# Performance work log

Hardware: AMD Instinct MI355X
Metric: run time of the kernel (lower is better)

The kernel has to match this reference:

```python
import jax, jax.numpy as jnp
import numpy as np

ALPHA = 1.702  # gpt-oss gated-activation alpha
LIMIT = 7.0    # gpt-oss clamp limit
E, H, I = 8, 1024, 2048
B, S = 2, 2048


def setup_inputs() -> dict:
    key = jax.random.key(0)
    ks = jax.random.split(key, 6)
    return {
        "hidden_states": jax.random.normal(ks[0], (B, S, H), dtype=jnp.float32),
        "routing_weights": jax.random.uniform(ks[1], (B * S, E), dtype=jnp.float32),
        "gate_up_proj": jax.random.normal(ks[2], (E, H, 2 * I), dtype=jnp.float32) * 0.02,
        "gate_up_proj_bias": jax.random.normal(ks[3], (E, 2 * I), dtype=jnp.float32) * 0.02,
        "down_proj": jax.random.normal(ks[4], (E, I, H), dtype=jnp.float32) * 0.02,
        "down_proj_bias": jax.random.normal(ks[5], (E, H), dtype=jnp.float32) * 0.02,
    }


def reference(hidden_states, routing_weights, gate_up_proj, gate_up_proj_bias,
              down_proj, down_proj_bias):
    b, s, h = hidden_states.shape
    x = hidden_states.reshape(-1, h)  # [T, H]
    # all-experts dense path: [E, T, 2I]
    gate_up = jnp.einsum('th,ehd->etd', x, gate_up_proj) + gate_up_proj_bias[:, None, :]
    gate = gate_up[..., ::2]   # interleaved gate/up as in gpt-oss
    up = gate_up[..., 1::2]
    gate = jnp.minimum(gate, LIMIT)
    up = jnp.clip(up, -LIMIT, LIMIT)
    glu = gate * jax.nn.sigmoid(gate * ALPHA)
    # [E, T, H]
    out_e = jnp.einsum('eti,eih->eth', (up + 1.0) * glu, down_proj) + down_proj_bias[:, None, :]
    # weighted sum over experts with routing weights [T, E]
    out = jnp.einsum('eth,te->th', out_e, routing_weights)
    return out.reshape(b, s, h)
```

## Files before the change

### kernel.cpp

```cpp
#include <hip/hip_runtime.h>
#include <cstdint>

#define E_  8
#define H_  1024
#define I_  2048
#define T_  4096
#define D2_ 4096
#define K2_ 16384

typedef __bf16 bf16x8 __attribute__((ext_vector_type(8)));
typedef float  f32x4  __attribute__((ext_vector_type(4)));

__device__ __forceinline__ unsigned short f2bf(float f) {
  unsigned int u = __float_as_uint(f);
  u += 0x7FFFu + ((u >> 16) & 1u);
  return (unsigned short)(u >> 16);
}

__device__ __forceinline__ void gll16(const void* g, void* l) {
  __builtin_amdgcn_global_load_lds(
      (const __attribute__((address_space(1))) unsigned int*)(uintptr_t)g,
      (__attribute__((address_space(3))) unsigned int*)(uintptr_t)l,
      16, 0, 0);
}

#define BARX()  __builtin_amdgcn_s_barrier()
#define FENCE() __builtin_amdgcn_sched_barrier(0)
#define LGK0()  asm volatile("s_waitcnt lgkmcnt(0)" ::: "memory")
#define WVM0()  asm volatile("s_waitcnt vmcnt(0)" ::: "memory")

__global__ void cast_x_kernel(const float* __restrict__ x,
                              unsigned short* __restrict__ xb) {
  const int idx = (blockIdx.x * 256 + threadIdx.x) * 8;
  float4 a = *(const float4*)(x + idx);
  float4 b = *(const float4*)(x + idx + 4);
  unsigned short o[8];
  o[0]=f2bf(a.x); o[1]=f2bf(a.y); o[2]=f2bf(a.z); o[3]=f2bf(a.w);
  o[4]=f2bf(b.x); o[5]=f2bf(b.y); o[6]=f2bf(b.z); o[7]=f2bf(b.w);
  *(uint4*)(xb + idx) = *(const uint4*)o;
}

__global__ void transp_w1_kernel(const float* __restrict__ gup,
                                 unsigned short* __restrict__ w1g,
                                 unsigned short* __restrict__ w1u) {
  __shared__ float tile[64][65];
  const int h0 = blockIdx.x * 64;
  const int d0 = blockIdx.y * 64;
  const int e  = blockIdx.z;
  const int tid = threadIdx.x;
  const int r  = tid >> 4;
  const int c4 = (tid & 15) * 4;
  const float* src = gup + ((size_t)e * H_ + h0) * D2_ + d0;
#pragma unroll
  for (int c = 0; c < 4; ++c) {
    const int row = r + 16 * c;
    float4 v = *(const float4*)(src + (size_t)row * D2_ + c4);
    tile[row][c4+0] = v.x; tile[row][c4+1] = v.y;
    tile[row][c4+2] = v.z; tile[row][c4+3] = v.w;
  }
  __syncthreads();
  const int hl = tid & 63;
  const int jg = tid >> 6;
  const size_t jbase = (size_t)e * I_ + (d0 >> 1);
#pragma unroll
  for (int jj = 0; jj < 8; ++jj) {
    const int jl = jg * 8 + jj;
    w1g[(jbase + jl) * H_ + h0 + hl] = f2bf(tile[hl][2*jl]);
    w1u[(jbase + jl) * H_ + h0 + hl] = f2bf(tile[hl][2*jl+1]);
  }
}

__global__ void transp_w2_kernel(const float* __restrict__ dp,
                                 unsigned short* __restrict__ w2t) {
  __shared__ float tile[64][65];
  const int k0 = blockIdx.x * 64;
  const int h0 = blockIdx.y * 64;
  const int tid = threadIdx.x;
  const int r  = tid >> 4;
  const int c4 = (tid & 15) * 4;
#pragma unroll
  for (int c = 0; c < 4; ++c) {
    const int row = r + 16 * c;
    float4 v = *(const float4*)(dp + (size_t)(k0 + row) * H_ + h0 + c4);
    tile[row][c4+0] = v.x; tile[row][c4+1] = v.y;
    tile[row][c4+2] = v.z; tile[row][c4+3] = v.w;
  }
  __syncthreads();
  const int kl = tid & 63;
  const int hg = tid >> 6;
#pragma unroll
  for (int hh = 0; hh < 16; ++hh) {
    const int hl = hg * 16 + hh;
    w2t[(size_t)(h0 + hl) * K2_ + k0 + kl] = f2bf(tile[kl][hl]);
  }
}


#define STA1(B, HF, KT) {                                                    \
  _Pragma("unroll")                                                           \
  for (int ld = 0; ld < 2; ++ld) {                                            \
    const int r = rA + (HF)*64 + ld*128;                                      \
    gll16(Ag + (size_t)r * H_ + (KT)*64 + sg, &lds[B][r*64 + sl]);            \
  } }
#define STG1(B, KT) {                                                         \
  _Pragma("unroll")                                                           \
  for (int ld = 0; ld < 2; ++ld) {                                            \
    const int r = rA + ld*64;                                                 \
    gll16(Gg + (size_t)r * H_ + (KT)*64 + sg, &lds[B][16384 + r*64 + sl]);    \
  } }
#define STU1(B, KT) {                                                         \
  _Pragma("unroll")                                                           \
  for (int ld = 0; ld < 2; ++ld) {                                            \
    const int r = rA + ld*64;                                                 \
    gll16(Ug + (size_t)r * H_ + (KT)*64 + sg, &lds[B][24576 + r*64 + sl]);    \
  } }
#define LDA1(B, MH) {                                                         \
  _Pragma("unroll")                                                           \
  for (int m = 0; m < 4; ++m) {                                               \
    const int ro = (wm*128 + (MH)*64 + m*16 + arow) * 64;                     \
    av[m][0] = *(const bf16x8*)&lds[B][ro + sw0];                             \
    av[m][1] = *(const bf16x8*)&lds[B][ro + sw1];                             \
  } }
#define LDB1(B, DST, BASE) {                                                  \
  _Pragma("unroll")                                                           \
  for (int n = 0; n < 2; ++n) {                                               \
    const int ro = (BASE) + (wn*32 + n*16 + arow) * 64;                       \
    DST[n][0] = *(const bf16x8*)&lds[B][ro + sw0];                            \
    DST[n][1] = *(const bf16x8*)&lds[B][ro + sw1];                            \
  } }
#define MMA1(ACC, MH, BV)                                                     \
  __builtin_amdgcn_s_setprio(1);                                              \
  _Pragma("unroll")                                                           \
  for (int m = 0; m < 4; ++m)                                                 \
  _Pragma("unroll")                                                           \
  for (int n = 0; n < 2; ++n) {                                               \
    ACC[(MH)*4+m][n] = __builtin_amdgcn_mfma_f32_16x16x32_bf16(av[m][0], BV[n][0], ACC[(MH)*4+m][n], 0,0,0); \
    ACC[(MH)*4+m][n] = __builtin_amdgcn_mfma_f32_16x16x32_bf16(av[m][1], BV[n][1], ACC[(MH)*4+m][n], 0,0,0); \
  }                                                                           \
  __builtin_amdgcn_s_setprio(0);

#define NT1 16
#define TILE1(B, U) {                                                         \
                \
  if ((U)+1 < NT1) { STA1((B)^1, 0, (U)+1); STA1((B)^1, 1, (U)+1);            \
                     STG1((B)^1, (U)+1);    STU1((B)^1, (U)+1); }             \
  FENCE();                          \
  LDA1(B, 0); LDB1(B, bgv, 16384); LDB1(B, buv, 24576);                       \
  MMA1(accg, 0, bgv); MMA1(accu, 0, buv);                                     \
  LDA1(B, 1);                                                                 \
  MMA1(accu, 1, buv); MMA1(accg, 1, bgv);                                     \
  LGK0();                      \
  if ((U)+1 < NT1) WVM0();       \
  BARX();                                                                     \
  FENCE();                                   \
}

__global__ __launch_bounds__(512, 2) void gemm1_act_kernel(
    const unsigned short* __restrict__ xb,
    const unsigned short* __restrict__ w1g,
    const unsigned short* __restrict__ w1u,
    const float* __restrict__ gub,
    const float* __restrict__ rw,
    unsigned short* __restrict__ actW)
{
  __shared__ unsigned short lds[2][32768];
  const int tid  = threadIdx.x;
  const int lane = tid & 63;
  const int wv   = tid >> 6;
  const int wm   = wv >> 2;
  const int wn   = wv & 3;

  const int L  = blockIdx.x + 16 * blockIdx.y;
  const int xk = L & 7, xs = L >> 3;
  const int t0 = ((xk >> 1) * 4 + (xs & 3)) * 256;
  const int j0 = ((xk & 1) * 8 + (xs >> 2)) * 128;
  const int e  = blockIdx.z;

  const int arow = lane & 15;
  const int q    = lane >> 4;
  const int sw0  = ((q    ) ^ (arow & 7)) * 8;
  const int sw1  = ((q + 4) ^ (arow & 7)) * 8;
  const int sg   = ((tid & 7) ^ ((tid >> 3) & 7)) * 8;
  const int sl   = (tid & 7) * 8;
  const int rA   = tid >> 3;

  const unsigned short* Ag = xb  + (size_t)t0 * H_;
  const unsigned short* Gg = w1g + ((size_t)e * I_ + j0) * H_;
  const unsigned short* Ug = w1u + ((size_t)e * I_ + j0) * H_;

  const f32x4 zero = {0.f, 0.f, 0.f, 0.f};
  f32x4 accg[8][2], accu[8][2];
#pragma unroll
  for (int m = 0; m < 8; ++m)
#pragma unroll
    for (int n = 0; n < 2; ++n) { accg[m][n] = zero; accu[m][n] = zero; }
  bf16x8 av[4][2], bgv[2][2], buv[2][2];

  STA1(0, 0, 0); STA1(0, 1, 0); STG1(0, 0); STU1(0, 0);
  WVM0(); BARX(); FENCE();

#pragma unroll 1
  for (int t = 0; t < NT1; t += 2) {
    TILE1(0, t);
    TILE1(1, t+1);
  }

  const float* gbE = gub + (size_t)e * D2_;
#pragma unroll
  for (int n = 0; n < 2; ++n) {
    const int j = j0 + wn*32 + n*16 + arow;
    const float2 bgu = *(const float2*)&gbE[2*j];
#pragma unroll
    for (int mf = 0; mf < 8; ++mf) {
#pragma unroll
      for (int ri = 0; ri < 4; ++ri) {
        const int t = t0 + wm*128 + mf*16 + q*4 + ri;
        float g = accg[mf][n][ri] + bgu.x;
        float u = accu[mf][n][ri] + bgu.y;
        g = fminf(g, 7.0f);
        u = fminf(fmaxf(u, -7.0f), 7.0f);
        const float s   = 1.0f / (1.0f + __expf(-1.702f * g));
        const float val = (u + 1.0f) * (g * s) * rw[t * 8 + e];
        actW[(size_t)t * K2_ + e * I_ + j] = f2bf(val);
      }
    }
  }
}


#define STA2(B, HF, KT) {                                                    \
  _Pragma("unroll")                                                           \
  for (int ld = 0; ld < 2; ++ld) {                                            \
    const int r = rA + (HF)*64 + ld*128;                                      \
    gll16(Ag + (size_t)r * K2_ + (KT)*64 + sg, &lds[B][r*64 + sl]);           \
  } }
#define STB2(B, NH, KT) {                                                    \
  _Pragma("unroll")                                                           \
  for (int ld = 0; ld < 2; ++ld) {                                            \
    const int lr = rA + ld*64;                                                \
    const int r  = (lr & 31) + (NH)*32 + ((lr >> 5) << 6);                    \
    gll16(Bgp + (size_t)r * K2_ + (KT)*64 + sg, &lds[B][16384 + r*64 + sl]);  \
  } }
#define LDA2(B, MH) {                                                         \
  _Pragma("unroll")                                                           \
  for (int m = 0; m < 4; ++m) {                                               \
    const int ro = (wm*128 + (MH)*64 + m*16 + arow) * 64;                     \
    av[m][0] = *(const bf16x8*)&lds[B][ro + sw0];                             \
    av[m][1] = *(const bf16x8*)&lds[B][ro + sw1];                             \
  } }
#define LDB2(B, DST, NH) {                                                   \
  _Pragma("unroll")                                                           \
  for (int n = 0; n < 2; ++n) {                                               \
    const int ro = 16384 + (wn*64 + (NH)*32 + n*16 + arow) * 64;              \
    DST[n][0] = *(const bf16x8*)&lds[B][ro + sw0];                            \
    DST[n][1] = *(const bf16x8*)&lds[B][ro + sw1];                            \
  } }
#define MMA2(MH, NH, BV)                                                      \
  __builtin_amdgcn_s_setprio(1);                                              \
  _Pragma("unroll")                                                           \
  for (int m = 0; m < 4; ++m)                                                 \
  _Pragma("unroll")                                                           \
  for (int n = 0; n < 2; ++n) {                                               \
    acc[(MH)*4+m][(NH)*2+n] = __builtin_amdgcn_mfma_f32_16x16x32_bf16(av[m][0], BV[n][0], acc[(MH)*4+m][(NH)*2+n], 0,0,0); \
    acc[(MH)*4+m][(NH)*2+n] = __builtin_amdgcn_mfma_f32_16x16x32_bf16(av[m][1], BV[n][1], acc[(MH)*4+m][(NH)*2+n], 0,0,0); \
  }                                                                           \
  __builtin_amdgcn_s_setprio(0);

#define NT2 64
#define TILE2(B, U) {                                                         \
  if ((U)+1 < NT2) { STA2((B)^1, 0, (U)+1); STA2((B)^1, 1, (U)+1);            \
                     STB2((B)^1, 0, (U)+1); STB2((B)^1, 1, (U)+1); }          \
  FENCE();                                                                    \
  LDA2(B, 0); LDB2(B, bv0, 0); LDB2(B, bv1, 1);                               \
  MMA2(0, 0, bv0); MMA2(0, 1, bv1);                                           \
  LDA2(B, 1);                                                                 \
  MMA2(1, 0, bv0); MMA2(1, 1, bv1);                                           \
  LGK0();                                                                     \
  if ((U)+1 < NT2) WVM0();                                                    \
  BARX();                                                                     \
  FENCE();                                                                    \
}

__global__ __launch_bounds__(512, 2) void gemm2_kernel(
    const unsigned short* __restrict__ actW,
    const unsigned short* __restrict__ w2t,
    float* __restrict__ part)
{
  __shared__ unsigned short lds[2][32768];
  const int tid  = threadIdx.x;
  const int lane = tid & 63;
  const int wv   = tid >> 6;
  const int wm   = wv >> 2;
  const int wn   = wv & 3;

  const int L  = blockIdx.x + 16 * (blockIdx.y + 4 * blockIdx.z);
  const int xk = L & 7, xs = L >> 3;
  const int t0 = ((xk & 1) * 8 + (xs & 7)) * 256;
  const int h0 = (xs >> 3) * 256;
  const int cz = xk >> 1;
  const int c0 = cz * 4096;

  const int arow = lane & 15;
  const int q    = lane >> 4;
  const int sw0  = ((q    ) ^ (arow & 7)) * 8;
  const int sw1  = ((q + 4) ^ (arow & 7)) * 8;
  const int sg   = ((tid & 7) ^ ((tid >> 3) & 7)) * 8;
  const int sl   = (tid & 7) * 8;
  const int rA   = tid >> 3;

  const unsigned short* Ag  = actW + (size_t)t0 * K2_ + c0;
  const unsigned short* Bgp = w2t  + (size_t)h0 * K2_ + c0;

  const f32x4 zero = {0.f, 0.f, 0.f, 0.f};
  f32x4 acc[8][4];
#pragma unroll
  for (int m = 0; m < 8; ++m)
#pragma unroll
    for (int n = 0; n < 4; ++n) acc[m][n] = zero;
  bf16x8 av[4][2], bv0[2][2], bv1[2][2];

  STA2(0, 0, 0); STA2(0, 1, 0); STB2(0, 0, 0); STB2(0, 1, 0);
  WVM0(); BARX(); FENCE();

#pragma unroll 1
  for (int t = 0; t < NT2; t += 2) {
    TILE2(0, t);
    TILE2(1, t+1);
  }

  float* P = part + (size_t)cz * ((size_t)T_ * H_);
#pragma unroll
  for (int mf = 0; mf < 8; ++mf)
#pragma unroll
    for (int nf = 0; nf < 4; ++nf)
#pragma unroll
      for (int ri = 0; ri < 4; ++ri) {
        const int t = t0 + wm*128 + mf*16 + q*4 + ri;
        const int h = h0 + wn*64 + nf*16 + arow;
        P[(size_t)t * H_ + h] = acc[mf][nf][ri];
      }
}

__global__ void reduce_kernel(const float* __restrict__ part,
                              const float* __restrict__ rw,
                              const float* __restrict__ dpb,
                              float* __restrict__ out) {
  const int idx = blockIdx.x * 256 + threadIdx.x;
  const int t  = idx >> 8;
  const int hq = idx & 255;
  const float4* p = (const float4*)part;
  float4 v = p[idx];
  float4 a;
  a = p[idx + 1048576]; v.x += a.x; v.y += a.y; v.z += a.z; v.w += a.w;
  a = p[idx + 2097152]; v.x += a.x; v.y += a.y; v.z += a.z; v.w += a.w;
  a = p[idx + 3145728]; v.x += a.x; v.y += a.y; v.z += a.z; v.w += a.w;
  const float4 w0 = *(const float4*)(rw + t*8);
  const float4 w1 = *(const float4*)(rw + t*8 + 4);
  const float wgt[8] = {w0.x, w0.y, w0.z, w0.w, w1.x, w1.y, w1.z, w1.w};
  const float4* db = (const float4*)dpb;
#pragma unroll
  for (int e2 = 0; e2 < 8; ++e2) {
    float4 b = db[e2*256 + hq];
    v.x += wgt[e2]*b.x; v.y += wgt[e2]*b.y; v.z += wgt[e2]*b.z; v.w += wgt[e2]*b.w;
  }
  ((float4*)out)[idx] = v;
}

extern "C" void kernel_launch(void* const* d_in, const int* in_sizes, int n_in,
                              void* d_out, int out_size, void* d_ws, size_t ws_size,
                              hipStream_t stream) {
  const float* hs  = (const float*)d_in[0];
  const float* rw  = (const float*)d_in[1];
  const float* gup = (const float*)d_in[2];
  const float* gub = (const float*)d_in[3];
  const float* dp  = (const float*)d_in[4];
  const float* dpb = (const float*)d_in[5];
  float* out = (float*)d_out;

  char* ws = (char*)d_ws;
  unsigned short* xb   = (unsigned short*)(ws);
  unsigned short* w1g  = (unsigned short*)(ws + 8388608);
  unsigned short* w1u  = (unsigned short*)(ws + 41943040);
  float*          part = (float*)(ws + 8388608);
  unsigned short* w2t  = (unsigned short*)(ws + 75497472);
  unsigned short* actW = (unsigned short*)(ws + 109051904);

  hipLaunchKernelGGL(cast_x_kernel, dim3((T_ * H_) / 2048), dim3(256), 0, stream, hs, xb);
  hipLaunchKernelGGL(transp_w1_kernel, dim3(H_/64, D2_/64, E_), dim3(256), 0, stream, gup, w1g, w1u);
  hipLaunchKernelGGL(transp_w2_kernel, dim3(K2_/64, H_/64), dim3(256), 0, stream, dp, w2t);
  hipLaunchKernelGGL(gemm1_act_kernel, dim3(T_/256, I_/128, E_), dim3(512), 0, stream,
                     xb, w1g, w1u, gub, rw, actW);
  hipLaunchKernelGGL(gemm2_kernel, dim3(T_/256, H_/256, 4), dim3(512), 0, stream,
                     actW, w2t, part);
  hipLaunchKernelGGL(reduce_kernel, dim3((T_ * H_ / 4) / 256), dim3(256), 0, stream,
                     part, rw, dpb, out);
}
```

Measured before the change: 439.1 us.

## Load B operands directly from global memory into registers, bypassing LDS

Both GEMM kernels now stage only the A (token) tile in LDS. Each wave reads its B-operand fragments (weights) straight from global memory into registers, which halves LDS usage and removes the B staging traffic. B is not shared across the wm warp rows, so each weight fragment is fetched twice, and those loads are issued without prefetch. The register loads sit on the critical path just before the MFMAs, which risks exposing global-memory latency.

Measured after the change: 694.2 us. +58.1%, slower.

```diff
diff --git a/kernel.cpp b/kernel.cpp
--- a/kernel.cpp
+++ b/kernel.cpp
@@ -102,18 +102,6 @@
     const int r = rA + (HF)*64 + ld*128;                                      \
     gll16(Ag + (size_t)r * H_ + (KT)*64 + sg, &lds[B][r*64 + sl]);            \
   } }
-#define STG1(B, KT) {                                                         \
-  _Pragma("unroll")                                                           \
-  for (int ld = 0; ld < 2; ++ld) {                                            \
-    const int r = rA + ld*64;                                                 \
-    gll16(Gg + (size_t)r * H_ + (KT)*64 + sg, &lds[B][16384 + r*64 + sl]);    \
-  } }
-#define STU1(B, KT) {                                                         \
-  _Pragma("unroll")                                                           \
-  for (int ld = 0; ld < 2; ++ld) {                                            \
-    const int r = rA + ld*64;                                                 \
-    gll16(Ug + (size_t)r * H_ + (KT)*64 + sg, &lds[B][24576 + r*64 + sl]);    \
-  } }
 #define LDA1(B, MH) {                                                         \
   _Pragma("unroll")                                                           \
   for (int m = 0; m < 4; ++m) {                                               \
@@ -121,12 +109,13 @@
     av[m][0] = *(const bf16x8*)&lds[B][ro + sw0];                             \
     av[m][1] = *(const bf16x8*)&lds[B][ro + sw1];                             \
   } }
-#define LDB1(B, DST, BASE) {                                                  \
+#define LDBG1(KT) {                                                           \
   _Pragma("unroll")                                                           \
   for (int n = 0; n < 2; ++n) {                                               \
-    const int ro = (BASE) + (wn*32 + n*16 + arow) * 64;                       \
-    DST[n][0] = *(const bf16x8*)&lds[B][ro + sw0];                            \
-    DST[n][1] = *(const bf16x8*)&lds[B][ro + sw1];                            \
+    const unsigned short* pg = Gg + (size_t)(wn*32 + n*16 + arow) * H_ + (KT)*64 + q*8; \
+    const unsigned short* pu = Ug + (size_t)(wn*32 + n*16 + arow) * H_ + (KT)*64 + q*8; \
+    bgv[n][0] = *(const bf16x8*)(pg);  bgv[n][1] = *(const bf16x8*)(pg + 32);  \
+    buv[n][0] = *(const bf16x8*)(pu);  buv[n][1] = *(const bf16x8*)(pu + 32);  \
   } }
 #define MMA1(ACC, MH, BV)                                                     \
   __builtin_amdgcn_s_setprio(1);                                              \
@@ -141,18 +130,17 @@
 
 #define NT1 16
 #define TILE1(B, U) {                                                         \
-                \
-  if ((U)+1 < NT1) { STA1((B)^1, 0, (U)+1); STA1((B)^1, 1, (U)+1);            \
-                     STG1((B)^1, (U)+1);    STU1((B)^1, (U)+1); }             \
-  FENCE();                          \
-  LDA1(B, 0); LDB1(B, bgv, 16384); LDB1(B, buv, 24576);                       \
+  LDBG1(U);                                        \
+  if ((U)+1 < NT1) { STA1((B)^1, 0, (U)+1); STA1((B)^1, 1, (U)+1); }          \
+  FENCE();                                                                    \
+  LDA1(B, 0);                                             \
   MMA1(accg, 0, bgv); MMA1(accu, 0, buv);                                     \
   LDA1(B, 1);                                                                 \
   MMA1(accu, 1, buv); MMA1(accg, 1, bgv);                                     \
-  LGK0();                      \
-  if ((U)+1 < NT1) WVM0();       \
+  LGK0();                                                                     \
+  if ((U)+1 < NT1) WVM0();   \
   BARX();                                                                     \
-  FENCE();                                   \
+  FENCE();                                                                    \
 }
 
 __global__ __launch_bounds__(512, 2) void gemm1_act_kernel(
@@ -163,7 +151,7 @@
     const float* __restrict__ rw,
     unsigned short* __restrict__ actW)
 {
-  __shared__ unsigned short lds[2][32768];
+  __shared__ unsigned short lds[2][16384];
   const int tid  = threadIdx.x;
   const int lane = tid & 63;
   const int wv   = tid >> 6;
@@ -196,7 +184,7 @@
     for (int n = 0; n < 2; ++n) { accg[m][n] = zero; accu[m][n] = zero; }
   bf16x8 av[4][2], bgv[2][2], buv[2][2];
 
-  STA1(0, 0, 0); STA1(0, 1, 0); STG1(0, 0); STU1(0, 0);
+  STA1(0, 0, 0); STA1(0, 1, 0);
   WVM0(); BARX(); FENCE();
 
 #pragma unroll 1
@@ -234,13 +222,6 @@
     const int r = rA + (HF)*64 + ld*128;                                      \
     gll16(Ag + (size_t)r * K2_ + (KT)*64 + sg, &lds[B][r*64 + sl]);           \
   } }
-#define STB2(B, NH, KT) {                                                    \
-  _Pragma("unroll")                                                           \
-  for (int ld = 0; ld < 2; ++ld) {                                            \
-    const int lr = rA + ld*64;                                                \
-    const int r  = (lr & 31) + (NH)*32 + ((lr >> 5) << 6);                    \
-    gll16(Bgp + (size_t)r * K2_ + (KT)*64 + sg, &lds[B][16384 + r*64 + sl]);  \
-  } }
 #define LDA2(B, MH) {                                                         \
   _Pragma("unroll")                                                           \
   for (int m = 0; m < 4; ++m) {                                               \
@@ -248,12 +229,13 @@
     av[m][0] = *(const bf16x8*)&lds[B][ro + sw0];                             \
     av[m][1] = *(const bf16x8*)&lds[B][ro + sw1];                             \
   } }
-#define LDB2(B, DST, NH) {                                                   \
+#define LDBG2(KT) {                                                           \
   _Pragma("unroll")                                                           \
   for (int n = 0; n < 2; ++n) {                                               \
-    const int ro = 16384 + (wn*64 + (NH)*32 + n*16 + arow) * 64;              \
-    DST[n][0] = *(const bf16x8*)&lds[B][ro + sw0];                            \
-    DST[n][1] = *(const bf16x8*)&lds[B][ro + sw1];                            \
+    const unsigned short* p0 = Bgp + (size_t)(wn*64 + n*16 + arow) * K2_ + (KT)*64 + q*8;      \
+    const unsigned short* p1 = Bgp + (size_t)(wn*64 + 32 + n*16 + arow) * K2_ + (KT)*64 + q*8; \
+    bv0[n][0] = *(const bf16x8*)(p0);  bv0[n][1] = *(const bf16x8*)(p0 + 32);  \
+    bv1[n][0] = *(const bf16x8*)(p1);  bv1[n][1] = *(const bf16x8*)(p1 + 32);  \
   } }
 #define MMA2(MH, NH, BV)                                                      \
   __builtin_amdgcn_s_setprio(1);                                              \
@@ -268,10 +250,10 @@
 
 #define NT2 64
 #define TILE2(B, U) {                                                         \
-  if ((U)+1 < NT2) { STA2((B)^1, 0, (U)+1); STA2((B)^1, 1, (U)+1);            \
-                     STB2((B)^1, 0, (U)+1); STB2((B)^1, 1, (U)+1); }          \
+  LDBG2(U);                                                                   \
+  if ((U)+1 < NT2) { STA2((B)^1, 0, (U)+1); STA2((B)^1, 1, (U)+1); }          \
   FENCE();                                                                    \
-  LDA2(B, 0); LDB2(B, bv0, 0); LDB2(B, bv1, 1);                               \
+  LDA2(B, 0);                                                                 \
   MMA2(0, 0, bv0); MMA2(0, 1, bv1);                                           \
   LDA2(B, 1);                                                                 \
   MMA2(1, 0, bv0); MMA2(1, 1, bv1);                                           \
@@ -286,7 +268,7 @@
     const unsigned short* __restrict__ w2t,
     float* __restrict__ part)
 {
-  __shared__ unsigned short lds[2][32768];
+  __shared__ unsigned short lds[2][16384];
   const int tid  = threadIdx.x;
   const int lane = tid & 63;
   const int wv   = tid >> 6;
@@ -319,7 +301,7 @@
     for (int n = 0; n < 4; ++n) acc[m][n] = zero;
   bf16x8 av[4][2], bv0[2][2], bv1[2][2];
 
-  STA2(0, 0, 0); STA2(0, 1, 0); STB2(0, 0, 0); STB2(0, 1, 0);
+  STA2(0, 0, 0); STA2(0, 1, 0);
   WVM0(); BARX(); FENCE();
 
 #pragma unroll 1
```
